# Optimization experiments

Hardware: AMD Instinct MI355X
Metric: run time of the kernel (lower is better)

## Reference

```python
import jax, jax.numpy as jnp
import numpy as np

B, N_IN, NV, F = 1, 65536, 1, 64
N_OUT, K = 16384, 16
N_DIST, N_PHI, OUT = 4, 8, 256
DIST_MAX = 0.1  # grid_layers[level_out].min_dist stand-in


def setup_inputs() -> dict:
    key = jax.random.key(0)
    ks = jax.random.split(key, 6)
    x = jax.random.normal(ks[0], (B, N_IN, NV, F), dtype=jnp.float32)
    nh_idx = jax.random.randint(ks[1], (N_OUT, K), 0, N_IN)  # neighbor gather indices
    d_dists = jax.random.uniform(ks[2], (N_OUT, K), dtype=jnp.float32) * DIST_MAX
    d_phi = jax.random.uniform(ks[3], (N_OUT, K), dtype=jnp.float32) * (2 * np.pi) - np.pi
    dists = jnp.linspace(0.0, DIST_MAX, N_DIST, dtype=jnp.float32)          # anchor distances
    sigma = jnp.asarray(DIST_MAX / 2, dtype=jnp.float32)                     # n_sigma == 1 -> scalar
    phi = jnp.linspace(-np.pi, np.pi, N_PHI + 1, dtype=jnp.float32)[:-1]     # von Mises: phi_min = -pi
    kappa = jnp.asarray(1.0, dtype=jnp.float32)                              # kappa_init
    W_out = jax.random.normal(ks[4], (F * N_DIST * N_PHI, OUT), dtype=jnp.float32) / np.sqrt(F * N_DIST * N_PHI)
    return {"x": x, "d_dists": d_dists, "d_phi": d_phi, "dists": dists,
            "sigma": sigma, "kappa": kappa, "phi": phi, "W_out": W_out, "nh_idx": nh_idx}


def reference(x, d_dists, d_phi, dists, sigma, kappa, phi, W_out, nh_idx):
    # Gaussian distance kernel: exp(-0.5*((d - dist_k)/sigma)^2)  -> (N_OUT, K, N_DIST)
    w_d = jnp.exp(-0.5 * ((d_dists[..., None] - dists) / sigma) ** 2)
    # von Mises angular kernel: exp(kappa * cos(d_phi - phi_p))   -> (N_OUT, K, N_PHI)
    w_p = jnp.exp(kappa * jnp.cos(d_phi[..., None] - phi))
    # combined kernel weights, normalized over the K neighbors per anchor
    w = w_d[..., :, None] * w_p[..., None, :]                      # (N_OUT, K, N_DIST, N_PHI)
    w = w / (jnp.sum(w, axis=1, keepdims=True) + 1e-9)
    w = w.reshape(N_OUT, K, N_DIST * N_PHI)                        # (N_OUT, K, M)
    # gather neighbor features from the input grid
    x_nb = x[:, nh_idx]                                            # (B, N_OUT, K, NV, F)
    # weighted aggregation over neighbors -> enhanced channels
    agg = jnp.einsum('bnkvf,nkm->bnvmf', x_nb, w)                  # (B, N_OUT, NV, M, F)
    agg = agg.reshape(B, N_OUT, NV, N_DIST * N_PHI * F)            # model_dim_enhanced = 2048
    return agg @ W_out                                             # (B, N_OUT, NV, OUT)
```

## Files before the change

kernel.cpp:

```cpp
#include <hip/hip_runtime.h>
#include <hip/hip_bf16.h>

#define N_IN   65536
#define N_OUTP 16384
#define KNB    16
#define FDIM   64
#define M_DIM  32
#define KDIM   2048
#define OUT_D  256

typedef __bf16 bf16x8_t __attribute__((ext_vector_type(8)));
typedef float  f32x4_t  __attribute__((ext_vector_type(4)));


__global__ __launch_bounds__(256) void pack_B_kernel(
    const float* __restrict__ W, uint4* __restrict__ Bws)
{
  int c    = blockIdx.x * 256 + threadIdx.x;
  int lane = c & 63;
  int nt   = (c >> 6) & 15;
  int kk   = c >> 10;
  int row0 = kk * 32 + (lane >> 4) * 8;
  int col  = nt * 16 + (lane & 15);
  union { unsigned short s[8]; uint4 v; } u;
#pragma unroll
  for (int j = 0; j < 8; ++j) {
    float f = W[(row0 + j) * OUT_D + col];
    __bf16 b = (__bf16)f;
    u.s[j] = __builtin_bit_cast(unsigned short, b);
  }
  Bws[c] = u.v;
}

#define AGG_ROWS 8
__global__ __launch_bounds__(256) void agg_kernel(
    const float* __restrict__ x,
    const float* __restrict__ d_dists,
    const float* __restrict__ d_phi,
    const float* __restrict__ dists,
    const float* __restrict__ sigma_p,
    const float* __restrict__ kappa_p,
    const float* __restrict__ phi,
    const int*   __restrict__ nh_idx,
    unsigned*    __restrict__ Aws)
{
  __shared__ float    wbuf[AGG_ROWS * 16 * 32];
  __shared__ float    winv[AGG_ROWS * 32];
  __shared__ int      idxb[AGG_ROWS * 16];
  __shared__ unsigned pkbuf[AGG_ROWS * 1028];

  const int t  = threadIdx.x;
  const int n0 = blockIdx.x * AGG_ROWS;
  const int T  = blockIdx.x >> 1;
  const int r0 = (blockIdx.x & 1) * 8;

  const float sinv = 1.0f / sigma_p[0];
  const float kap  = kappa_p[0];
  float phiv[8], distv[4];
#pragma unroll
  for (int p = 0; p < 8; ++p) phiv[p] = phi[p];
#pragma unroll
  for (int d = 0; d < 4; ++d) distv[d] = dists[d];

  {
    int rk = t >> 1, r8 = rk >> 4, k = rk & 15, rep = t & 1;
    int n = n0 + r8;
    float dd = d_dists[n * KNB + k];
    float dp = d_phi[n * KNB + k];
    float wp[8];
#pragma unroll
    for (int p = 0; p < 8; ++p) wp[p] = __expf(kap * __cosf(dp - phiv[p]));
#pragma unroll
    for (int dl = 0; dl < 2; ++dl) {
      int d = rep * 2 + dl;
      float td = (dd - distv[d]) * sinv;
      float wd = __expf(-0.5f * td * td);
      float4 w0 = make_float4(wd * wp[0], wd * wp[1], wd * wp[2], wd * wp[3]);
      float4 w1 = make_float4(wd * wp[4], wd * wp[5], wd * wp[6], wd * wp[7]);
      float* dst = wbuf + (r8 * 16 + k) * 32 + d * 8;
      *(float4*)(dst)     = w0;
      *(float4*)(dst + 4) = w1;
    }
    if (t < 128) {
      int r8b = t >> 4, kb = t & 15;
      idxb[r8b * 16 + kb] = nh_idx[(n0 + r8b) * KNB + kb];
    }
  }
  __syncthreads();

  {
    int r8 = t >> 5, m = t & 31;
    float s = 0.f;
#pragma unroll
    for (int k = 0; k < 16; ++k) s += wbuf[(r8 * 16 + k) * 32 + m];
    winv[r8 * 32 + m] = 1.0f / (s + 1e-9f);
  }
  __syncthreads();

  {
    int fg = t & 31, r8 = t >> 5;
    float acc0[32], acc1[32];
#pragma unroll
    for (int m = 0; m < 32; ++m) { acc0[m] = 0.f; acc1[m] = 0.f; }
    const float2* xp = (const float2*)x;
#pragma unroll
    for (int k = 0; k < 16; ++k) {
      int idx = idxb[r8 * 16 + k];
      float2 xv = xp[idx * 32 + fg];
      const float4* wrow4 = (const float4*)(wbuf + (r8 * 16 + k) * 32);
#pragma unroll
      for (int mm = 0; mm < 8; ++mm) {
        float4 wv = wrow4[mm];
        acc0[mm * 4 + 0] += wv.x * xv.x;  acc1[mm * 4 + 0] += wv.x * xv.y;
        acc0[mm * 4 + 1] += wv.y * xv.x;  acc1[mm * 4 + 1] += wv.y * xv.y;
        acc0[mm * 4 + 2] += wv.z * xv.x;  acc1[mm * 4 + 2] += wv.z * xv.y;
        acc0[mm * 4 + 3] += wv.w * xv.x;  acc1[mm * 4 + 3] += wv.w * xv.y;
      }
    }
#pragma unroll
    for (int m = 0; m < 32; ++m) {
      float wn = winv[r8 * 32 + m];
      __bf16 b0 = (__bf16)(acc0[m] * wn);
      __bf16 b1 = (__bf16)(acc1[m] * wn);
      unsigned pk = ((unsigned)__builtin_bit_cast(unsigned short, b1) << 16)
                  |  (unsigned)__builtin_bit_cast(unsigned short, b0);
      pkbuf[r8 * 1028 + m * 32 + fg] = pk;
    }
  }
  __syncthreads();

  {
    int b   = t & 3;
    int rr  = (t >> 2) & 7;
    int ks  = (t >> 5) & 3;
    int kks = t >> 7;
    unsigned* g = Aws + (size_t)T * 16384 + ks * 64 + (r0 + rr) * 4 + b;
    const unsigned* src = pkbuf + rr * 1028 + ks * 4 + b;
#pragma unroll
    for (int i = 0; i < 32; ++i) {
      int kk = kks * 32 + i;
      g[kk * 256] = src[kk * 16];
    }
  }
}

__global__ __launch_bounds__(512) void gemm_kernel(
    const uint4* __restrict__ Astream,
    const uint4* __restrict__ Bws,
    float*       __restrict__ out)
{
  const int t    = threadIdx.x;
  const int lane = t & 63;
  const int w    = t >> 6;
  const int rb   = blockIdx.x;

  const uint4* pa = Astream + (size_t)(rb * 4 + (w & 1) * 2) * 4096 + lane;
  const uint4* pb = Bws + ((w >> 1) * 4) * 64 + lane;

  f32x4_t cacc[2][4];
#pragma unroll
  for (int mt = 0; mt < 2; ++mt)
#pragma unroll
    for (int i = 0; i < 4; ++i)
      cacc[mt][i] = (f32x4_t){0.f, 0.f, 0.f, 0.f};

  uint4 a[2][2], b[2][4];
#pragma unroll
  for (int s = 0; s < 2; ++s) {
    a[s][0] = pa[s * 64];
    a[s][1] = pa[4096 + s * 64];
#pragma unroll
    for (int i = 0; i < 4; ++i) b[s][i] = pb[s * 1024 + i * 64];
  }

#pragma unroll 4
  for (int kk = 0; kk < 64; ++kk) {
    const int s = kk & 1;
    bf16x8_t A0 = __builtin_bit_cast(bf16x8_t, a[s][0]);
    bf16x8_t A1 = __builtin_bit_cast(bf16x8_t, a[s][1]);
#pragma unroll
    for (int i = 0; i < 4; ++i) {
      bf16x8_t B = __builtin_bit_cast(bf16x8_t, b[s][i]);
      cacc[0][i] = __builtin_amdgcn_mfma_f32_16x16x32_bf16(A0, B, cacc[0][i], 0, 0, 0);
      cacc[1][i] = __builtin_amdgcn_mfma_f32_16x16x32_bf16(A1, B, cacc[1][i], 0, 0, 0);
    }
    if (kk < 62) {
      a[s][0] = pa[(kk + 2) * 64];
      a[s][1] = pa[4096 + (kk + 2) * 64];
#pragma unroll
      for (int i = 0; i < 4; ++i) b[s][i] = pb[(kk + 2) * 1024 + i * 64];
    }
  }

  const int rbase = rb * 64 + (w & 1) * 32 + (lane >> 4) * 4;
  const int cbase = (w >> 1) * 64 + (lane & 15);
#pragma unroll
  for (int mt = 0; mt < 2; ++mt)
#pragma unroll
    for (int i = 0; i < 4; ++i)
#pragma unroll
      for (int reg = 0; reg < 4; ++reg)
        out[(rbase + mt * 16 + reg) * OUT_D + cbase + i * 16] = cacc[mt][i][reg];
}

extern "C" void kernel_launch(void* const* d_in, const int* in_sizes, int n_in,
                              void* d_out, int out_size, void* d_ws, size_t ws_size,
                              hipStream_t stream) {
  const float* x      = (const float*)d_in[0];
  const float* dd     = (const float*)d_in[1];
  const float* dp     = (const float*)d_in[2];
  const float* dists  = (const float*)d_in[3];
  const float* sigma  = (const float*)d_in[4];
  const float* kappa  = (const float*)d_in[5];
  const float* phi    = (const float*)d_in[6];
  const float* W      = (const float*)d_in[7];
  const int*   nh     = (const int*)d_in[8];
  float*       out    = (float*)d_out;

  uint4* Bws = (uint4*)d_ws;
  uint4* Aws = (uint4*)((char*)d_ws + (1 << 20));

  pack_B_kernel<<<256, 256, 0, stream>>>(W, Bws);
  agg_kernel<<<N_OUTP / AGG_ROWS, 256, 0, stream>>>(
      x, dd, dp, dists, sigma, kappa, phi, nh, (unsigned*)Aws);
  gemm_kernel<<<N_OUTP / 64, 512, 0, stream>>>(Aws, Bws, out);
}
```

Measured before the change: 71.97 us.

## Stage gathered neighbor features in LDS and use 8x8 register tiles in aggregation

The aggregation kernel now copies the gathered x rows for each block into padded shared memory with float4 loads, replacing the per-thread float2 global gathers. Each thread then computes an 8x8 (m, f) outer-product tile from LDS, which raises arithmetic intensity per LDS read compared with the previous 32x2 layout. The x staging buffer is aliased with the bf16 pack buffer, which needs an extra barrier, and the pack writes are rotated per m-group to reduce bank conflicts. The goal is better memory coalescing and fewer LDS reads per FMA, at the cost of more shared memory and an added synchronization.

```diff
diff --git a/kernel.cpp b/kernel.cpp
--- a/kernel.cpp
+++ b/kernel.cpp
@@ -33,6 +33,9 @@
 }
 
 #define AGG_ROWS 8
+#define XK  68
+#define XR8 (16 * XK)
+
 __global__ __launch_bounds__(256) void agg_kernel(
     const float* __restrict__ x,
     const float* __restrict__ d_dists,
@@ -44,10 +47,12 @@
     const int*   __restrict__ nh_idx,
     unsigned*    __restrict__ Aws)
 {
-  __shared__ float    wbuf[AGG_ROWS * 16 * 32];
-  __shared__ float    winv[AGG_ROWS * 32];
-  __shared__ int      idxb[AGG_ROWS * 16];
-  __shared__ unsigned pkbuf[AGG_ROWS * 1028];
+  __shared__ float wbuf[AGG_ROWS * 16 * 32];
+  __shared__ float winv[AGG_ROWS * 32];
+  __shared__ int   idxb[AGG_ROWS * 16];
+  __shared__ __align__(16) char xpk_raw[AGG_ROWS * XR8 * 4];
+  float*    xbuf  = (float*)xpk_raw;
+  unsigned* pkbuf = (unsigned*)xpk_raw;
 
   const int t  = threadIdx.x;
   const int n0 = blockIdx.x * AGG_ROWS;
@@ -89,6 +94,14 @@
   __syncthreads();
 
   {
+    int h = t & 1, k = (t >> 1) & 15, r8 = t >> 5;
+    int idx = idxb[r8 * 16 + k];
+    const float4* xr = (const float4*)x + (size_t)idx * 16 + h * 8;
+    float4* xd = (float4*)(xbuf + r8 * XR8 + k * XK + h * 36);
+#pragma unroll
+    for (int j = 0; j < 8; ++j) xd[j] = xr[j];
+  }
+  {
     int r8 = t >> 5, m = t & 31;
     float s = 0.f;
 #pragma unroll
@@ -97,34 +110,53 @@
   }
   __syncthreads();
 
-  {
-    int fg = t & 31, r8 = t >> 5;
-    float acc0[32], acc1[32];
-#pragma unroll
-    for (int m = 0; m < 32; ++m) { acc0[m] = 0.f; acc1[m] = 0.f; }
-    const float2* xp = (const float2*)x;
+  float acc[8][8];
+  const int fg = t & 7, mg = (t >> 3) & 3, r8 = t >> 5;
+  {
+#pragma unroll
+    for (int mi = 0; mi < 8; ++mi)
+#pragma unroll
+      for (int fi = 0; fi < 8; ++fi) acc[mi][fi] = 0.f;
+
+    const float* wp_ = wbuf + r8 * 512 + mg * 8;
+    const float* xp_ = xbuf + r8 * XR8 + ((fg < 4) ? fg * 8 : 36 + (fg - 4) * 8);
+
 #pragma unroll
     for (int k = 0; k < 16; ++k) {
-      int idx = idxb[r8 * 16 + k];
-      float2 xv = xp[idx * 32 + fg];
-      const float4* wrow4 = (const float4*)(wbuf + (r8 * 16 + k) * 32);
-#pragma unroll
-      for (int mm = 0; mm < 8; ++mm) {
-        float4 wv = wrow4[mm];
-        acc0[mm * 4 + 0] += wv.x * xv.x;  acc1[mm * 4 + 0] += wv.x * xv.y;
-        acc0[mm * 4 + 1] += wv.y * xv.x;  acc1[mm * 4 + 1] += wv.y * xv.y;
-        acc0[mm * 4 + 2] += wv.z * xv.x;  acc1[mm * 4 + 2] += wv.z * xv.y;
-        acc0[mm * 4 + 3] += wv.w * xv.x;  acc1[mm * 4 + 3] += wv.w * xv.y;
+      float4 wa = *(const float4*)(wp_ + k * 32);
+      float4 wb = *(const float4*)(wp_ + k * 32 + 4);
+      float4 xa = *(const float4*)(xp_ + k * XK);
+      float4 xb = *(const float4*)(xp_ + k * XK + 4);
+      float wv[8] = {wa.x, wa.y, wa.z, wa.w, wb.x, wb.y, wb.z, wb.w};
+      float xv[8] = {xa.x, xa.y, xa.z, xa.w, xb.x, xb.y, xb.z, xb.w};
+#pragma unroll
+      for (int mi = 0; mi < 8; ++mi)
+#pragma unroll
+        for (int fi = 0; fi < 8; ++fi)
+          acc[mi][fi] += wv[mi] * xv[fi];
+    }
+#pragma unroll
+    for (int mi = 0; mi < 8; ++mi) {
+      float wn = winv[r8 * 32 + mg * 8 + mi];
+#pragma unroll
+      for (int fi = 0; fi < 8; ++fi) acc[mi][fi] *= wn;
+    }
+  }
+  __syncthreads();
+
+  {
+    unsigned* pb = pkbuf + r8 * 1028 + (mg * 8) * 32 + fg * 4;
+#pragma unroll
+    for (int jj = 0; jj < 4; ++jj) {
+      int fi2 = (jj + mg) & 3;
+#pragma unroll
+      for (int mi = 0; mi < 8; ++mi) {
+        __bf16 b0 = (__bf16)acc[mi][fi2 * 2];
+        __bf16 b1 = (__bf16)acc[mi][fi2 * 2 + 1];
+        unsigned pk = ((unsigned)__builtin_bit_cast(unsigned short, b1) << 16)
+                    |  (unsigned)__builtin_bit_cast(unsigned short, b0);
+        pb[mi * 32 + fi2] = pk;
       }
-    }
-#pragma unroll
-    for (int m = 0; m < 32; ++m) {
-      float wn = winv[r8 * 32 + m];
-      __bf16 b0 = (__bf16)(acc0[m] * wn);
-      __bf16 b1 = (__bf16)(acc1[m] * wn);
-      unsigned pk = ((unsigned)__builtin_bit_cast(unsigned short, b1) << 16)
-                  |  (unsigned)__builtin_bit_cast(unsigned short, b0);
-      pkbuf[r8 * 1028 + m * 32 + fg] = pk;
     }
   }
   __syncthreads();
```

Result: slower. 112.2 us (+55.9%).

## Stage gathered rows in LDS, register-tile aggregation, and deepen GEMM prefetch

Applied to the files above, without the earlier changes.

The aggregation kernel now issues the neighbor gather up front as coalesced float4 loads into registers, before the weight computation, and stages the rows in padded LDS. The weights are normalized in place, so the inner product becomes an 8x8 register-tiled outer product that writes packed bf16 uint4 directly to the GEMM A layout. This removes the pkbuf staging pass, one barrier and the scattered 32-bit stores. The GEMM register prefetch depth goes from 2 to 4 stages, which raises register pressure.

```diff
diff --git a/kernel.cpp b/kernel.cpp
--- a/kernel.cpp
+++ b/kernel.cpp
@@ -12,6 +12,12 @@
 typedef __bf16 bf16x8_t __attribute__((ext_vector_type(8)));
 typedef float  f32x4_t  __attribute__((ext_vector_type(4)));
 
+
+__device__ __forceinline__ unsigned pk2(float a, float b) {
+  __bf16 b0 = (__bf16)a, b1 = (__bf16)b;
+  return ((unsigned)__builtin_bit_cast(unsigned short, b1) << 16) |
+          (unsigned)__builtin_bit_cast(unsigned short, b0);
+}
 
 __global__ __launch_bounds__(256) void pack_B_kernel(
     const float* __restrict__ W, uint4* __restrict__ Bws)
@@ -32,7 +38,11 @@
   Bws[c] = u.v;
 }
 
-#define AGG_ROWS 8
+#define WST 580
+#define WKS 36
+#define XST 1092
+#define XKS 68
+
 __global__ __launch_bounds__(256) void agg_kernel(
     const float* __restrict__ x,
     const float* __restrict__ d_dists,
@@ -42,27 +52,32 @@
     const float* __restrict__ kappa_p,
     const float* __restrict__ phi,
     const int*   __restrict__ nh_idx,
-    unsigned*    __restrict__ Aws)
+    uint4*       __restrict__ Aws)
 {
-  __shared__ float    wbuf[AGG_ROWS * 16 * 32];
-  __shared__ float    winv[AGG_ROWS * 32];
-  __shared__ int      idxb[AGG_ROWS * 16];
-  __shared__ unsigned pkbuf[AGG_ROWS * 1028];
+  __shared__ __align__(16) float wbuf[8 * WST];
+  __shared__ __align__(16) float xbuf[8 * XST];
 
   const int t  = threadIdx.x;
-  const int n0 = blockIdx.x * AGG_ROWS;
+  const int n0 = blockIdx.x * 8;
   const int T  = blockIdx.x >> 1;
   const int r0 = (blockIdx.x & 1) * 8;
 
-  const float sinv = 1.0f / sigma_p[0];
-  const float kap  = kappa_p[0];
-  float phiv[8], distv[4];
-#pragma unroll
-  for (int p = 0; p < 8; ++p) phiv[p] = phi[p];
-#pragma unroll
-  for (int d = 0; d < 4; ++d) distv[d] = dists[d];
-
-  {
+  const int h = t & 1, gk = (t >> 1) & 15, gr8 = t >> 5;
+  const int gidx = nh_idx[(n0 + gr8) * KNB + gk];
+  const float4* xr = (const float4*)x + (size_t)gidx * 16 + h * 8;
+  float4 xreg[8];
+#pragma unroll
+  for (int j = 0; j < 8; ++j) xreg[j] = xr[j];
+
+  {
+    const float sinv = 1.0f / sigma_p[0];
+    const float kap  = kappa_p[0];
+    float phiv[8], distv[4];
+#pragma unroll
+    for (int p = 0; p < 8; ++p) phiv[p] = phi[p];
+#pragma unroll
+    for (int d = 0; d < 4; ++d) distv[d] = dists[d];
+
     int rk = t >> 1, r8 = rk >> 4, k = rk & 15, rep = t & 1;
     int n = n0 + r8;
     float dd = d_dists[n * KNB + k];
@@ -75,71 +90,72 @@
       int d = rep * 2 + dl;
       float td = (dd - distv[d]) * sinv;
       float wd = __expf(-0.5f * td * td);
-      float4 w0 = make_float4(wd * wp[0], wd * wp[1], wd * wp[2], wd * wp[3]);
-      float4 w1 = make_float4(wd * wp[4], wd * wp[5], wd * wp[6], wd * wp[7]);
-      float* dst = wbuf + (r8 * 16 + k) * 32 + d * 8;
-      *(float4*)(dst)     = w0;
-      *(float4*)(dst + 4) = w1;
-    }
-    if (t < 128) {
-      int r8b = t >> 4, kb = t & 15;
-      idxb[r8b * 16 + kb] = nh_idx[(n0 + r8b) * KNB + kb];
-    }
+      float* dst = wbuf + r8 * WST + k * WKS + d * 8;
+      *(float4*)(dst)     = make_float4(wd * wp[0], wd * wp[1], wd * wp[2], wd * wp[3]);
+      *(float4*)(dst + 4) = make_float4(wd * wp[4], wd * wp[5], wd * wp[6], wd * wp[7]);
+    }
+  }
+
+  {
+    float4* xd = (float4*)(xbuf + gr8 * XST + gk * XKS + h * 36);
+#pragma unroll
+    for (int j = 0; j < 8; ++j) xd[j] = xreg[j];
   }
   __syncthreads();
 
   {
     int r8 = t >> 5, m = t & 31;
+    float wv[16];
     float s = 0.f;
 #pragma unroll
-    for (int k = 0; k < 16; ++k) s += wbuf[(r8 * 16 + k) * 32 + m];
-    winv[r8 * 32 + m] = 1.0f / (s + 1e-9f);
+    for (int k = 0; k < 16; ++k) {
+      wv[k] = wbuf[r8 * WST + k * WKS + m];
+      s += wv[k];
+    }
+    float wn = 1.0f / (s + 1e-9f);
+#pragma unroll
+    for (int k = 0; k < 16; ++k)
+      wbuf[r8 * WST + k * WKS + m] = wv[k] * wn;
   }
   __syncthreads();
 
   {
-    int fg = t & 31, r8 = t >> 5;
-    float acc0[32], acc1[32];
-#pragma unroll
-    for (int m = 0; m < 32; ++m) { acc0[m] = 0.f; acc1[m] = 0.f; }
-    const float2* xp = (const float2*)x;
-#pragma unroll
+    const int r8 = t & 7, fo = (t >> 3) & 7, mq = t >> 6;
+    float acc[8][8];
+#pragma unroll
+    for (int mi = 0; mi < 8; ++mi)
+#pragma unroll
+      for (int fi = 0; fi < 8; ++fi) acc[mi][fi] = 0.f;
+
+    const float* wp_ = wbuf + r8 * WST + mq * 8;
+    const float* xp_ = xbuf + r8 * XST + ((fo < 4) ? fo * 8 : 36 + (fo - 4) * 8);
+
+#pragma unroll 4
     for (int k = 0; k < 16; ++k) {
-      int idx = idxb[r8 * 16 + k];
-      float2 xv = xp[idx * 32 + fg];
-      const float4* wrow4 = (const float4*)(wbuf + (r8 * 16 + k) * 32);
-#pragma unroll
-      for (int mm = 0; mm < 8; ++mm) {
-        float4 wv = wrow4[mm];
-        acc0[mm * 4 + 0] += wv.x * xv.x;  acc1[mm * 4 + 0] += wv.x * xv.y;
-        acc0[mm * 4 + 1] += wv.y * xv.x;  acc1[mm * 4 + 1] += wv.y * xv.y;
-        acc0[mm * 4 + 2] += wv.z * xv.x;  acc1[mm * 4 + 2] += wv.z * xv.y;
-        acc0[mm * 4 + 3] += wv.w * xv.x;  acc1[mm * 4 + 3] += wv.w * xv.y;
-      }
-    }
-#pragma unroll
-    for (int m = 0; m < 32; ++m) {
-      float wn = winv[r8 * 32 + m];
-      __bf16 b0 = (__bf16)(acc0[m] * wn);
-      __bf16 b1 = (__bf16)(acc1[m] * wn);
-      unsigned pk = ((unsigned)__builtin_bit_cast(unsigned short, b1) << 16)
-                  |  (unsigned)__builtin_bit_cast(unsigned short, b0);
-      pkbuf[r8 * 1028 + m * 32 + fg] = pk;
-    }
-  }
-  __syncthreads();
-
-  {
-    int b   = t & 3;
-    int rr  = (t >> 2) & 7;
-    int ks  = (t >> 5) & 3;
-    int kks = t >> 7;
-    unsigned* g = Aws + (size_t)T * 16384 + ks * 64 + (r0 + rr) * 4 + b;
-    const unsigned* src = pkbuf + rr * 1028 + ks * 4 + b;
-#pragma unroll
-    for (int i = 0; i < 32; ++i) {
-      int kk = kks * 32 + i;
-      g[kk * 256] = src[kk * 16];
+      float4 wa = *(const float4*)(wp_ + k * WKS);
+      float4 wb = *(const float4*)(wp_ + k * WKS + 4);
+      float4 xa = *(const float4*)(xp_ + k * XKS);
+      float4 xb = *(const float4*)(xp_ + k * XKS + 4);
+      float wv[8] = {wa.x, wa.y, wa.z, wa.w, wb.x, wb.y, wb.z, wb.w};
+      float xv[8] = {xa.x, xa.y, xa.z, xa.w, xb.x, xb.y, xb.z, xb.w};
+#pragma unroll
+      for (int mi = 0; mi < 8; ++mi)
+#pragma unroll
+        for (int fi = 0; fi < 8; ++fi)
+          acc[mi][fi] += wv[mi] * xv[fi];
+    }
+
+    uint4* base = Aws + (size_t)T * 4096 + (fo & 3) * 16 + r0 + r8
+                      + (size_t)(fo >> 2) * 64;
+#pragma unroll
+    for (int mi = 0; mi < 8; ++mi) {
+      int m = mq * 8 + mi;
+      uint4 v;
+      v.x = pk2(acc[mi][0], acc[mi][1]);
+      v.y = pk2(acc[mi][2], acc[mi][3]);
+      v.z = pk2(acc[mi][4], acc[mi][5]);
+      v.w = pk2(acc[mi][6], acc[mi][7]);
+      base[m * 128] = v;
     }
   }
 }
@@ -164,9 +180,9 @@
     for (int i = 0; i < 4; ++i)
       cacc[mt][i] = (f32x4_t){0.f, 0.f, 0.f, 0.f};
 
-  uint4 a[2][2], b[2][4];
-#pragma unroll
-  for (int s = 0; s < 2; ++s) {
+  uint4 a[4][2], b[4][4];
+#pragma unroll
+  for (int s = 0; s < 4; ++s) {
     a[s][0] = pa[s * 64];
     a[s][1] = pa[4096 + s * 64];
 #pragma unroll
@@ -175,7 +191,7 @@
 
 #pragma unroll 4
   for (int kk = 0; kk < 64; ++kk) {
-    const int s = kk & 1;
+    const int s = kk & 3;
     bf16x8_t A0 = __builtin_bit_cast(bf16x8_t, a[s][0]);
     bf16x8_t A1 = __builtin_bit_cast(bf16x8_t, a[s][1]);
 #pragma unroll
@@ -184,11 +200,11 @@
       cacc[0][i] = __builtin_amdgcn_mfma_f32_16x16x32_bf16(A0, B, cacc[0][i], 0, 0, 0);
       cacc[1][i] = __builtin_amdgcn_mfma_f32_16x16x32_bf16(A1, B, cacc[1][i], 0, 0, 0);
     }
-    if (kk < 62) {
-      a[s][0] = pa[(kk + 2) * 64];
-      a[s][1] = pa[4096 + (kk + 2) * 64];
-#pragma unroll
-      for (int i = 0; i < 4; ++i) b[s][i] = pb[(kk + 2) * 1024 + i * 64];
+    if (kk < 60) {
+      a[s][0] = pa[(kk + 4) * 64];
+      a[s][1] = pa[4096 + (kk + 4) * 64];
+#pragma unroll
+      for (int i = 0; i < 4; ++i) b[s][i] = pb[(kk + 4) * 1024 + i * 64];
     }
   }
 
@@ -221,7 +237,7 @@
   uint4* Aws = (uint4*)((char*)d_ws + (1 << 20));
 
   pack_B_kernel<<<256, 256, 0, stream>>>(W, Bws);
-  agg_kernel<<<N_OUTP / AGG_ROWS, 256, 0, stream>>>(
-      x, dd, dp, dists, sigma, kappa, phi, nh, (unsigned*)Aws);
+  agg_kernel<<<N_OUTP / 8, 256, 0, stream>>>(
+      x, dd, dp, dists, sigma, kappa, phi, nh, Aws);
   gemm_kernel<<<N_OUTP / 64, 512, 0, stream>>>(Aws, Bws, out);
 }
```

New measurement: 64.95 us. -9.8%, faster.
